# Optimization experiments

Measured on AMD Instinct MI355X. Metric: run time of the kernel, lower is better.

The kernel has to match this reference:

```python
import jax, jax.numpy as jnp
import numpy as np

DIM = 64
SQRT_DIM = float(np.sqrt(DIM))


def setup_inputs() -> dict:
    key = jax.random.key(0)
    k1, k2, k3, k4 = jax.random.split(key, 4)
    B, S, D = 32, 2048, DIM
    query = jax.random.normal(k1, (B, S, D), dtype=jnp.float32)
    key_t = jax.random.normal(k2, (B, S, D), dtype=jnp.float32)
    value = jax.random.normal(k3, (B, S, D), dtype=jnp.float32)
    mask = jax.random.randint(k4, (B, S, S), 0, 2).astype(jnp.bool_)
    return {"query": query, "key": key_t, "value": value, "mask": mask}


def reference(query, key, value, mask):
    # score: [B, S, S]
    score = jnp.einsum('bqd,bkd->bqk', query, key) / SQRT_DIM
    score = jnp.where(mask, -jnp.inf, score)
    attn = jax.nn.softmax(score, axis=-1)
    # fully-masked rows produce NaN in softmax; torch.nan_to_num -> 0
    attn = jnp.nan_to_num(attn, nan=0.0)
    context = jnp.einsum('bqk,bkd->bqd', attn, value)
    return context
```

## Files before the change

### kernel.cpp

```cpp
#include <hip/hip_runtime.h>
#include <hip/hip_bf16.h>

#define BATCH 32
#define SEQ   2048
#define DIM   64
#define KT    32
#define NIT   (SEQ / KT)

typedef __attribute__((ext_vector_type(8))) short bf16x8;
typedef __attribute__((ext_vector_type(4))) short bf16x4;
typedef __attribute__((ext_vector_type(4))) float fx4;
typedef __attribute__((ext_vector_type(4))) int   ix4;

static __device__ __forceinline__ short f2bf(float f) {
    __bf16 h = (__bf16)f;
    return *(short*)&h;
}
static __device__ __forceinline__ bf16x8 cvt8(fx4 a, fx4 b) {
    bf16x8 s;
    s[0] = f2bf(a[0]); s[1] = f2bf(a[1]); s[2] = f2bf(a[2]); s[3] = f2bf(a[3]);
    s[4] = f2bf(b[0]); s[5] = f2bf(b[1]); s[6] = f2bf(b[2]); s[7] = f2bf(b[3]);
    return s;
}
static __device__ __forceinline__ bf16x4 cvt4(float a, float b, float c, float d) {
    bf16x4 s; s[0] = f2bf(a); s[1] = f2bf(b); s[2] = f2bf(c); s[3] = f2bf(d);
    return s;
}

#define QSCALE (0.125f * 1.44269504088896f)

__global__ __launch_bounds__(1024, 4)
void attn_fwd(const float* __restrict__ Qg, const float* __restrict__ Kg,
              const float* __restrict__ Vg, const int* __restrict__ Mg,
              float* __restrict__ Og)
{
    __shared__ __align__(16) char smem[16384];

    const int bid   = (int)((blockIdx.x & 7) * 32 + (blockIdx.x >> 3));
    const int b     = bid >> 3;
    const int qbase = (bid & 7) * 256;
    const int tid   = threadIdx.x;
    const int wave  = tid >> 6;
    const int lane  = tid & 63;
    const int l15   = lane & 15;
    const int g     = lane >> 4;

    const int qrow_g = qbase + wave * 16 + l15;
    const float* qrow = Qg + ((size_t)(b * SEQ + qrow_g) * DIM);
    bf16x8 qf[2];
#pragma unroll
    for (int h = 0; h < 2; ++h) {
        fx4 a = *(const fx4*)(qrow + h * 32 + g * 8);
        fx4 c = *(const fx4*)(qrow + h * 32 + g * 8 + 4);
        a *= QSCALE; c *= QSCALE;
        qf[h] = cvt8(a, c);
    }

    const int* mrow = Mg + ((size_t)(b * SEQ + qrow_g) * SEQ) + 4 * g;

    const bool isK = tid < 512;
    const int kr = (tid & 511) >> 4, kcq = tid & 15;
    const float* ksrc = Kg + ((size_t)(b * SEQ + kr) * DIM) + kcq * 4;
    const int kwofs = kr * 128 + ((kcq * 8) ^ ((kr & 7) * 16));
    const int t2 = tid & 511;
    const int vd = t2 & 63, jg = t2 >> 6;
    const float* vsrc = Vg + ((size_t)(b * SEQ + jg * 4) * DIM) + vd;
    const int vpr = vd >> 1, vu = vd & 1;
    const int vwofs = 8192 + vpr * 128 +
                      (((vu * 64) + 16 * (jg & 3) + 8 * (jg >> 2)) ^ ((vpr & 7) * 16));

    const int ksw = (l15 & 7) * 16;
    const int kofs00 = (l15)      * 128 + ((16 * g)      ^ ksw);
    const int kofs01 = (l15)      * 128 + ((16 * g + 64) ^ ksw);
    const int kofs10 = (16 + l15) * 128 + ((16 * g)      ^ ksw);
    const int kofs11 = (16 + l15) * 128 + ((16 * g + 64) ^ ksw);
    const int vofs = 8192 + (l15 >> 1) * 128 + (((l15 & 1) * 64 + 16 * g) ^ ((l15 >> 1) * 16));

    fx4 acc[4] = {};
    float lsum = 0.f;

    fx4   kReg[2];
    float vReg[2][4];
    ix4 mA0, mA1, mB0, mB1;

    if (isK) {
        fx4 k0 = *(const fx4*)(ksrc);
        kReg[0] = *(const fx4*)(ksrc + (size_t)KT * DIM);
        *(bf16x4*)(smem + kwofs) = cvt4(k0[0], k0[1], k0[2], k0[3]);
    } else {
        float v0[4];
#pragma unroll
        for (int i = 0; i < 4; ++i) v0[i] = vsrc[(size_t)i * DIM];
#pragma unroll
        for (int i = 0; i < 4; ++i) vReg[0][i] = vsrc[(size_t)(KT + i) * DIM];
        *(bf16x4*)(smem + vwofs) = cvt4(v0[0], v0[1], v0[2], v0[3]);
    }
    mA0 = __builtin_nontemporal_load((const ix4*)(mrow));
    mA1 = __builtin_nontemporal_load((const ix4*)(mrow + 16));
    mB0 = __builtin_nontemporal_load((const ix4*)(mrow + KT));
    mB1 = __builtin_nontemporal_load((const ix4*)(mrow + KT + 16));
    asm volatile("s_waitcnt lgkmcnt(0)" ::: "memory");
    __builtin_amdgcn_s_barrier();
    __builtin_amdgcn_sched_barrier(0);

#pragma unroll 2
    for (int kt = 0; kt < NIT; ++kt) {
        const int cur = kt & 1, nxt = cur ^ 1;
        const int kb2 = ((kt + 2) & (NIT - 1)) * KT;

        if (isK) {
            kReg[nxt] = *(const fx4*)(ksrc + (size_t)kb2 * DIM);
        } else {
#pragma unroll
            for (int i = 0; i < 4; ++i) vReg[nxt][i] = vsrc[(size_t)(kb2 + i) * DIM];
        }

        ix4 mC0 = __builtin_nontemporal_load((const ix4*)(mrow + kb2));
        ix4 mC1 = __builtin_nontemporal_load((const ix4*)(mrow + kb2 + 16));

        const char* kb_ = smem + cur * 4096;
        fx4 s0 = {}, s1 = {};
        {
            bf16x8 kf;
            kf = *(const bf16x8*)(kb_ + kofs00); s0 = __builtin_amdgcn_mfma_f32_16x16x32_bf16(kf, qf[0], s0, 0, 0, 0);
            kf = *(const bf16x8*)(kb_ + kofs01); s0 = __builtin_amdgcn_mfma_f32_16x16x32_bf16(kf, qf[1], s0, 0, 0, 0);
            kf = *(const bf16x8*)(kb_ + kofs10); s1 = __builtin_amdgcn_mfma_f32_16x16x32_bf16(kf, qf[0], s1, 0, 0, 0);
            kf = *(const bf16x8*)(kb_ + kofs11); s1 = __builtin_amdgcn_mfma_f32_16x16x32_bf16(kf, qf[1], s1, 0, 0, 0);
        }
        float p[8];
        p[0] = mA0[0] ? 0.f : __builtin_amdgcn_exp2f(s0[0]);
        p[1] = mA0[1] ? 0.f : __builtin_amdgcn_exp2f(s0[1]);
        p[2] = mA0[2] ? 0.f : __builtin_amdgcn_exp2f(s0[2]);
        p[3] = mA0[3] ? 0.f : __builtin_amdgcn_exp2f(s0[3]);
        p[4] = mA1[0] ? 0.f : __builtin_amdgcn_exp2f(s1[0]);
        p[5] = mA1[1] ? 0.f : __builtin_amdgcn_exp2f(s1[1]);
        p[6] = mA1[2] ? 0.f : __builtin_amdgcn_exp2f(s1[2]);
        p[7] = mA1[3] ? 0.f : __builtin_amdgcn_exp2f(s1[3]);
        lsum += ((p[0] + p[1]) + (p[2] + p[3])) + ((p[4] + p[5]) + (p[6] + p[7]));
        bf16x8 pf;
#pragma unroll
        for (int j = 0; j < 8; ++j) pf[j] = f2bf(p[j]);

        const char* vb_ = smem + cur * 4096;
#pragma unroll
        for (int dsub = 0; dsub < 4; ++dsub) {
            bf16x8 vf = *(const bf16x8*)(vb_ + vofs + dsub * 1024);
            acc[dsub] = __builtin_amdgcn_mfma_f32_16x16x32_bf16(vf, pf, acc[dsub], 0, 0, 0);
        }

        if (isK) {
            *(bf16x4*)(smem + nxt * 4096 + kwofs) =
                cvt4(kReg[cur][0], kReg[cur][1], kReg[cur][2], kReg[cur][3]);
        } else {
            *(bf16x4*)(smem + nxt * 4096 + vwofs) =
                cvt4(vReg[cur][0], vReg[cur][1], vReg[cur][2], vReg[cur][3]);
        }

        mA0 = mB0; mA1 = mB1; mB0 = mC0; mB1 = mC1;

        asm volatile("s_waitcnt lgkmcnt(0)" ::: "memory");
        __builtin_amdgcn_s_barrier();
        __builtin_amdgcn_sched_barrier(0);
    }

    lsum += __shfl_xor(lsum, 16);
    lsum += __shfl_xor(lsum, 32);
    const float inv = lsum > 0.f ? 1.0f / lsum : 0.f;

    float* obase = Og + ((size_t)(b * SEQ + qrow_g) * DIM) + 4 * g;
#pragma unroll
    for (int dsub = 0; dsub < 4; ++dsub) {
        fx4 o = acc[dsub] * inv;
        __builtin_nontemporal_store(o, (fx4*)(obase + dsub * 16));
    }
}

extern "C" void kernel_launch(void* const* d_in, const int* in_sizes, int n_in,
                              void* d_out, int out_size, void* d_ws, size_t ws_size,
                              hipStream_t stream) {
    const float* Q = (const float*)d_in[0];
    const float* K = (const float*)d_in[1];
    const float* V = (const float*)d_in[2];
    const int*   M = (const int*)d_in[3];
    float*       O = (float*)d_out;
    dim3 grid(BATCH * (SEQ / 256));
    attn_fwd<<<grid, 1024, 0, stream>>>(Q, K, V, M, O);
}
```

Before: 144.5 us.

## Double key tile to 64 and have every thread stage both K and V

Raises the key tile from 32 to 64, so each iteration runs twice as many MFMAs per barrier and the loop makes half as many trips. All 1024 threads now load and convert both K and V instead of splitting the work between halves of the block, and LDS doubles to 32KB. The mask prefetch changes from two tiles ahead to one tile ahead with four vector loads per thread. This amortizes barrier and loop overhead, but it adds register pressure and shortens the distance the mask load has to hide latency.

Result: faster. 136.3 us (-5.7%).

```diff
diff --git a/kernel.cpp b/kernel.cpp
--- a/kernel.cpp
+++ b/kernel.cpp
@@ -4,8 +4,9 @@
 #define BATCH 32
 #define SEQ   2048
 #define DIM   64
-#define KT    32
+#define KT    64
 #define NIT   (SEQ / KT)
+#define QTB   256
 
 typedef __attribute__((ext_vector_type(8))) short bf16x8;
 typedef __attribute__((ext_vector_type(4))) short bf16x4;
@@ -15,12 +16,6 @@
 static __device__ __forceinline__ short f2bf(float f) {
     __bf16 h = (__bf16)f;
     return *(short*)&h;
-}
-static __device__ __forceinline__ bf16x8 cvt8(fx4 a, fx4 b) {
-    bf16x8 s;
-    s[0] = f2bf(a[0]); s[1] = f2bf(a[1]); s[2] = f2bf(a[2]); s[3] = f2bf(a[3]);
-    s[4] = f2bf(b[0]); s[5] = f2bf(b[1]); s[6] = f2bf(b[2]); s[7] = f2bf(b[3]);
-    return s;
 }
 static __device__ __forceinline__ bf16x4 cvt4(float a, float b, float c, float d) {
     bf16x4 s; s[0] = f2bf(a); s[1] = f2bf(b); s[2] = f2bf(c); s[3] = f2bf(d);
@@ -34,11 +29,11 @@
               const float* __restrict__ Vg, const int* __restrict__ Mg,
               float* __restrict__ Og)
 {
-    __shared__ __align__(16) char smem[16384];
+    __shared__ __align__(16) char smem[32768];
 
     const int bid   = (int)((blockIdx.x & 7) * 32 + (blockIdx.x >> 3));
     const int b     = bid >> 3;
-    const int qbase = (bid & 7) * 256;
+    const int qbase = (bid & 7) * QTB;
     const int tid   = threadIdx.x;
     const int wave  = tid >> 6;
     const int lane  = tid & 63;
@@ -53,52 +48,50 @@
         fx4 a = *(const fx4*)(qrow + h * 32 + g * 8);
         fx4 c = *(const fx4*)(qrow + h * 32 + g * 8 + 4);
         a *= QSCALE; c *= QSCALE;
-        qf[h] = cvt8(a, c);
+        bf16x8 q;
+        q[0]=f2bf(a[0]); q[1]=f2bf(a[1]); q[2]=f2bf(a[2]); q[3]=f2bf(a[3]);
+        q[4]=f2bf(c[0]); q[5]=f2bf(c[1]); q[6]=f2bf(c[2]); q[7]=f2bf(c[3]);
+        qf[h] = q;
     }
 
     const int* mrow = Mg + ((size_t)(b * SEQ + qrow_g) * SEQ) + 4 * g;
 
-    const bool isK = tid < 512;
-    const int kr = (tid & 511) >> 4, kcq = tid & 15;
+    const int kr = tid >> 4, kcq = tid & 15;
     const float* ksrc = Kg + ((size_t)(b * SEQ + kr) * DIM) + kcq * 4;
     const int kwofs = kr * 128 + ((kcq * 8) ^ ((kr & 7) * 16));
-    const int t2 = tid & 511;
-    const int vd = t2 & 63, jg = t2 >> 6;
+
+    const int vd = tid & 63, jg = tid >> 6;
     const float* vsrc = Vg + ((size_t)(b * SEQ + jg * 4) * DIM) + vd;
-    const int vpr = vd >> 1, vu = vd & 1;
-    const int vwofs = 8192 + vpr * 128 +
-                      (((vu * 64) + 16 * (jg & 3) + 8 * (jg >> 2)) ^ ((vpr & 7) * 16));
+    const int vpr = vd >> 1, vu = vd & 1, jg7 = jg & 7;
+    const int vwofs = 16384 + (jg >> 3) * 4096 + vpr * 128 +
+                      (((vu * 64) + 16 * (jg7 & 3) + 8 * (jg7 >> 2)) ^ ((vpr & 7) * 16));
 
-    const int ksw = (l15 & 7) * 16;
-    const int kofs00 = (l15)      * 128 + ((16 * g)      ^ ksw);
-    const int kofs01 = (l15)      * 128 + ((16 * g + 64) ^ ksw);
-    const int kofs10 = (16 + l15) * 128 + ((16 * g)      ^ ksw);
-    const int kofs11 = (16 + l15) * 128 + ((16 * g + 64) ^ ksw);
-    const int vofs = 8192 + (l15 >> 1) * 128 + (((l15 & 1) * 64 + 16 * g) ^ ((l15 >> 1) * 16));
+    const int ksw  = (l15 & 7) * 16;
+    const int koh0 = l15 * 128 + ((16 * g)      ^ ksw);
+    const int koh1 = l15 * 128 + ((16 * g + 64) ^ ksw);
+    const int vrof = (l15 >> 1) * 128 + (((l15 & 1) * 64 + 16 * g) ^ ((l15 >> 1) * 16));
 
     fx4 acc[4] = {};
     float lsum = 0.f;
 
     fx4   kReg[2];
     float vReg[2][4];
-    ix4 mA0, mA1, mB0, mB1;
+    ix4   m[4];
 
-    if (isK) {
+    {
         fx4 k0 = *(const fx4*)(ksrc);
-        kReg[0] = *(const fx4*)(ksrc + (size_t)KT * DIM);
-        *(bf16x4*)(smem + kwofs) = cvt4(k0[0], k0[1], k0[2], k0[3]);
-    } else {
         float v0[4];
 #pragma unroll
         for (int i = 0; i < 4; ++i) v0[i] = vsrc[(size_t)i * DIM];
+        kReg[0] = *(const fx4*)(ksrc + (size_t)KT * DIM);
 #pragma unroll
         for (int i = 0; i < 4; ++i) vReg[0][i] = vsrc[(size_t)(KT + i) * DIM];
+#pragma unroll
+        for (int s = 0; s < 4; ++s)
+            m[s] = __builtin_nontemporal_load((const ix4*)(mrow + s * 16));
+        *(bf16x4*)(smem + kwofs) = cvt4(k0[0], k0[1], k0[2], k0[3]);
         *(bf16x4*)(smem + vwofs) = cvt4(v0[0], v0[1], v0[2], v0[3]);
     }
-    mA0 = __builtin_nontemporal_load((const ix4*)(mrow));
-    mA1 = __builtin_nontemporal_load((const ix4*)(mrow + 16));
-    mB0 = __builtin_nontemporal_load((const ix4*)(mrow + KT));
-    mB1 = __builtin_nontemporal_load((const ix4*)(mrow + KT + 16));
     asm volatile("s_waitcnt lgkmcnt(0)" ::: "memory");
     __builtin_amdgcn_s_barrier();
     __builtin_amdgcn_sched_barrier(0);
@@ -107,56 +100,57 @@
     for (int kt = 0; kt < NIT; ++kt) {
         const int cur = kt & 1, nxt = cur ^ 1;
         const int kb2 = ((kt + 2) & (NIT - 1)) * KT;
+        const int kb1 = ((kt + 1) & (NIT - 1)) * KT;
 
-        if (isK) {
-            kReg[nxt] = *(const fx4*)(ksrc + (size_t)kb2 * DIM);
-        } else {
+        kReg[nxt] = *(const fx4*)(ksrc + (size_t)kb2 * DIM);
 #pragma unroll
-            for (int i = 0; i < 4; ++i) vReg[nxt][i] = vsrc[(size_t)(kb2 + i) * DIM];
+        for (int i = 0; i < 4; ++i) vReg[nxt][i] = vsrc[(size_t)(kb2 + i) * DIM];
+
+        const char* kB = smem + cur * 8192;
+        fx4 sc[4];
+#pragma unroll
+        for (int s = 0; s < 4; ++s) {
+            bf16x8 kf0 = *(const bf16x8*)(kB + s * 2048 + koh0);
+            bf16x8 kf1 = *(const bf16x8*)(kB + s * 2048 + koh1);
+            fx4 t = {};
+            t = __builtin_amdgcn_mfma_f32_16x16x32_bf16(kf0, qf[0], t, 0, 0, 0);
+            t = __builtin_amdgcn_mfma_f32_16x16x32_bf16(kf1, qf[1], t, 0, 0, 0);
+            sc[s] = t;
         }
 
-        ix4 mC0 = __builtin_nontemporal_load((const ix4*)(mrow + kb2));
-        ix4 mC1 = __builtin_nontemporal_load((const ix4*)(mrow + kb2 + 16));
+        float p[16];
+#pragma unroll
+        for (int s = 0; s < 4; ++s)
+#pragma unroll
+            for (int i = 0; i < 4; ++i)
+                p[s * 4 + i] = m[s][i] ? 0.f : __builtin_amdgcn_exp2f(sc[s][i]);
+#pragma unroll
+        for (int s = 0; s < 4; ++s)
+            m[s] = __builtin_nontemporal_load((const ix4*)(mrow + kb1 + s * 16));
 
-        const char* kb_ = smem + cur * 4096;
-        fx4 s0 = {}, s1 = {};
-        {
-            bf16x8 kf;
-            kf = *(const bf16x8*)(kb_ + kofs00); s0 = __builtin_amdgcn_mfma_f32_16x16x32_bf16(kf, qf[0], s0, 0, 0, 0);
-            kf = *(const bf16x8*)(kb_ + kofs01); s0 = __builtin_amdgcn_mfma_f32_16x16x32_bf16(kf, qf[1], s0, 0, 0, 0);
-            kf = *(const bf16x8*)(kb_ + kofs10); s1 = __builtin_amdgcn_mfma_f32_16x16x32_bf16(kf, qf[0], s1, 0, 0, 0);
-            kf = *(const bf16x8*)(kb_ + kofs11); s1 = __builtin_amdgcn_mfma_f32_16x16x32_bf16(kf, qf[1], s1, 0, 0, 0);
-        }
-        float p[8];
-        p[0] = mA0[0] ? 0.f : __builtin_amdgcn_exp2f(s0[0]);
-        p[1] = mA0[1] ? 0.f : __builtin_amdgcn_exp2f(s0[1]);
-        p[2] = mA0[2] ? 0.f : __builtin_amdgcn_exp2f(s0[2]);
-        p[3] = mA0[3] ? 0.f : __builtin_amdgcn_exp2f(s0[3]);
-        p[4] = mA1[0] ? 0.f : __builtin_amdgcn_exp2f(s1[0]);
-        p[5] = mA1[1] ? 0.f : __builtin_amdgcn_exp2f(s1[1]);
-        p[6] = mA1[2] ? 0.f : __builtin_amdgcn_exp2f(s1[2]);
-        p[7] = mA1[3] ? 0.f : __builtin_amdgcn_exp2f(s1[3]);
-        lsum += ((p[0] + p[1]) + (p[2] + p[3])) + ((p[4] + p[5]) + (p[6] + p[7]));
-        bf16x8 pf;
+        lsum += (((p[0] + p[1]) + (p[2] + p[3])) + ((p[4] + p[5]) + (p[6] + p[7])))
+              + (((p[8] + p[9]) + (p[10] + p[11])) + ((p[12] + p[13]) + (p[14] + p[15])));
+
+        bf16x8 pf0, pf1;
 #pragma unroll
-        for (int j = 0; j < 8; ++j) pf[j] = f2bf(p[j]);
+        for (int j = 0; j < 8; ++j) { pf0[j] = f2bf(p[j]); pf1[j] = f2bf(p[8 + j]); }
 
-        const char* vb_ = smem + cur * 4096;
+        const char* vB = smem + 16384 + cur * 8192 + vrof;
 #pragma unroll
         for (int dsub = 0; dsub < 4; ++dsub) {
-            bf16x8 vf = *(const bf16x8*)(vb_ + vofs + dsub * 1024);
-            acc[dsub] = __builtin_amdgcn_mfma_f32_16x16x32_bf16(vf, pf, acc[dsub], 0, 0, 0);
+            bf16x8 vf = *(const bf16x8*)(vB + dsub * 1024);
+            acc[dsub] = __builtin_amdgcn_mfma_f32_16x16x32_bf16(vf, pf0, acc[dsub], 0, 0, 0);
+        }
+#pragma unroll
+        for (int dsub = 0; dsub < 4; ++dsub) {
+            bf16x8 vf = *(const bf16x8*)(vB + 4096 + dsub * 1024);
+            acc[dsub] = __builtin_amdgcn_mfma_f32_16x16x32_bf16(vf, pf1, acc[dsub], 0, 0, 0);
         }
 
-        if (isK) {
-            *(bf16x4*)(smem + nxt * 4096 + kwofs) =
-                cvt4(kReg[cur][0], kReg[cur][1], kReg[cur][2], kReg[cur][3]);
-        } else {
-            *(bf16x4*)(smem + nxt * 4096 + vwofs) =
-                cvt4(vReg[cur][0], vReg[cur][1], vReg[cur][2], vReg[cur][3]);
-        }
-
-        mA0 = mB0; mA1 = mB1; mB0 = mC0; mB1 = mC1;
+        *(bf16x4*)(smem + nxt * 8192 + kwofs) =
+            cvt4(kReg[cur][0], kReg[cur][1], kReg[cur][2], kReg[cur][3]);
+        *(bf16x4*)(smem + nxt * 8192 + vwofs) =
+            cvt4(vReg[cur][0], vReg[cur][1], vReg[cur][2], vReg[cur][3]);
 
         asm volatile("s_waitcnt lgkmcnt(0)" ::: "memory");
         __builtin_amdgcn_s_barrier();
@@ -183,6 +177,6 @@
     const float* V = (const float*)d_in[2];
     const int*   M = (const int*)d_in[3];
     float*       O = (float*)d_out;
-    dim3 grid(BATCH * (SEQ / 256));
+    dim3 grid(BATCH * (SEQ / QTB));
     attn_fwd<<<grid, 1024, 0, stream>>>(Q, K, V, M, O);
 }
```
